# Performance work log

Measured on AMD Instinct MI355X. Metric: run time of the kernel, lower is better.

## Reference

```python
import jax, jax.numpy as jnp
import numpy as np

N, S, H, D = 2, 1024, 12, 64
HIDDEN = H * D
EPS = 1e-6


def setup_inputs() -> dict:
    key = jax.random.key(0)
    k1, k2, k3 = jax.random.split(key, 3)
    return {
        "q": jax.random.normal(k1, (N, S, H, D), dtype=jnp.float32),
        "v": jax.random.normal(k2, (N, S, H, D), dtype=jnp.float32),
        "attention_mask": jnp.ones((N, S), dtype=jnp.float32),
        "head_mask": jnp.ones((H,), dtype=jnp.float32),
        "pos_weight": jax.random.normal(k3, (S, HIDDEN), dtype=jnp.float32),
    }


def reference(q, v, attention_mask, head_mask, pos_weight):
    seq_len = q.shape[1]
    # transpose_for_scores: [S, hidden] -> [S, H, D]
    p = pos_weight[:seq_len].reshape(seq_len, H, D)
    # elu feature map: elu(x) + 1
    p = jax.nn.elu(p) + 1.0
    # broadcast to batch and apply padding mask: [N, S, H, D]
    p = p[None, :, :, :] * attention_mask[:, :, None, None]
    # pv: [N, H, M, D]
    pv = jnp.einsum('nshd,nshm->nhmd', p, v)
    pv = pv * head_mask[None, :, None, None]
    # ppv: [N, L, H, M, D]
    ppv = jnp.einsum('nlhd,nhmd->nlhmd', p, pv)
    # normalizer z_pp: [N, L, H]
    z_pp = jnp.einsum('nlhd,nhd->nlh', p, p.sum(axis=1)) + EPS
    return ppv, z_pp
```

## Files before the change

kernel.cpp:

```cpp
#include <hip/hip_runtime.h>
#include <math.h>

#define N_  2
#define S_  1024
#define H_  12
#define D_  64
#define HIDDEN_ 768
#define EPS_ 1e-6f

#define CHUNK 64
#define NS    (S_/CHUNK)

__device__ __forceinline__ float elup1(float x) {
    return x > 0.0f ? x + 1.0f : __expf(x);
}

__global__ __launch_bounds__(256) void pv_kernel(
        const float* __restrict__ v,
        const float* __restrict__ mask,
        const float* __restrict__ w,
        float* __restrict__ pv_part,
        float* __restrict__ psum_part) {
    __shared__ float p_lds[CHUNK * 64];
    __shared__ float v_lds[CHUNK * 64];

    const int b  = blockIdx.x;
    const int sc = b % NS;
    const int h  = (b / NS) % H_;
    const int n  = b / (NS * H_);
    const int s0 = sc * CHUNK;
    const int t  = threadIdx.x;

    for (int j = t; j < CHUNK * 16; j += 256) {
        const int row = j >> 4;
        const int c4  = (j & 15) * 4;
        const int s   = s0 + row;
        const float m = mask[n * S_ + s];
        const float4 wv = *(const float4*)(w + (size_t)s * HIDDEN_ + h * 64 + c4);
        float4 p;
        p.x = elup1(wv.x) * m;
        p.y = elup1(wv.y) * m;
        p.z = elup1(wv.z) * m;
        p.w = elup1(wv.w) * m;
        *(float4*)(p_lds + row * 64 + c4) = p;
        const float4 vv = *(const float4*)(v + (((size_t)n * S_ + s) * H_ + h) * 64 + c4);
        *(float4*)(v_lds + row * 64 + c4) = vv;
    }
    __syncthreads();

    const int d  = t & 63;
    const int mq = t >> 6;
    float acc[16];
    #pragma unroll
    for (int i = 0; i < 16; ++i) acc[i] = 0.0f;
    float ps = 0.0f;

    for (int s = 0; s < CHUNK; ++s) {
        const float pd = p_lds[s * 64 + d];
        ps += pd;
        const float* vr = v_lds + s * 64 + mq * 16;
        #pragma unroll
        for (int i = 0; i < 16; ++i)
            acc[i] = fmaf(pd, vr[i], acc[i]);
    }

    float* pvp = pv_part + (((size_t)(n * H_ + h)) * NS + sc) * (64 * 64);
    #pragma unroll
    for (int i = 0; i < 16; ++i)
        pvp[(mq * 16 + i) * 64 + d] = acc[i];
    if (mq == 0)
        psum_part[(((size_t)(n * H_ + h)) * NS + sc) * 64 + d] = ps;
}

__global__ __launch_bounds__(256) void reduce_kernel(
        const float* __restrict__ pv_part,
        const float* __restrict__ psum_part,
        float* __restrict__ pv_ws,
        float* __restrict__ psum_ws) {
    const int nh = blockIdx.x;
    const int t  = threadIdx.x;
    const float* src = pv_part + (size_t)nh * NS * 4096;
    float* dst = pv_ws + (size_t)nh * 4096;

    #pragma unroll
    for (int k = 0; k < 16; ++k) {
        const int e = t + k * 256;
        float s = 0.0f;
        #pragma unroll
        for (int sc = 0; sc < NS; ++sc)
            s += src[(size_t)sc * 4096 + e];
        dst[e] = s;
    }
    if (t < 64) {
        const float* ps = psum_part + (size_t)nh * NS * 64;
        float s = 0.0f;
        #pragma unroll
        for (int sc = 0; sc < NS; ++sc)
            s += ps[sc * 64 + t];
        psum_ws[nh * 64 + t] = s;
    }
}

__global__ __launch_bounds__(256) void ppv_kernel(
        const float* __restrict__ w,
        const float* __restrict__ mask,
        const float* __restrict__ head_mask,
        const float* __restrict__ pv_ws,
        const float* __restrict__ psum_ws,
        float* __restrict__ ppv_out,
        float* __restrict__ z_out) {
    __shared__ float p_l[64];

    const int b = blockIdx.x;
    const int h = b % H_;
    const int l = (b / H_) % S_;
    const int n = b / (H_ * S_);
    const int t = threadIdx.x;

    if (t < 64) {
        const float x = w[(size_t)l * HIDDEN_ + h * 64 + t];
        const float m = mask[n * S_ + l];
        const float p = elup1(x) * m;
        p_l[t] = p;
        float pz = p * psum_ws[(n * H_ + h) * 64 + t];
        #pragma unroll
        for (int off = 32; off > 0; off >>= 1)
            pz += __shfl_down(pz, off, 64);
        if (t == 0) z_out[b] = pz + EPS_;
    }
    __syncthreads();

    const float hm = head_mask[h];
    const float4* pv4 = (const float4*)(pv_ws + ((size_t)n * H_ + h) * (64 * 64));
    float4* out4 = (float4*)(ppv_out + (size_t)b * (64 * 64));

    #pragma unroll
    for (int jj = 0; jj < 4; ++jj) {
        const int j = t + jj * 256;
        const float4 vv = pv4[j];
        const float4 pw = *(const float4*)(p_l + ((j * 4) & 63));
        float4 r;
        r.x = pw.x * vv.x * hm;
        r.y = pw.y * vv.y * hm;
        r.z = pw.z * vv.z * hm;
        r.w = pw.w * vv.w * hm;
        out4[j] = r;
    }
}

extern "C" void kernel_launch(void* const* d_in, const int* in_sizes, int n_in,
                              void* d_out, int out_size, void* d_ws, size_t ws_size,
                              hipStream_t stream) {
    const float* v     = (const float*)d_in[1];
    const float* mask  = (const float*)d_in[2];
    const float* hmask = (const float*)d_in[3];
    const float* w     = (const float*)d_in[4];
    float* out = (float*)d_out;

    float* pv_part   = (float*)d_ws;
    float* psum_part = pv_part + (size_t)N_ * H_ * NS * 64 * 64;
    float* pv_ws     = psum_part + (size_t)N_ * H_ * NS * 64;
    float* psum_ws   = pv_ws + (size_t)N_ * H_ * 64 * 64;

    pv_kernel<<<dim3(N_ * H_ * NS), dim3(256), 0, stream>>>(
        v, mask, w, pv_part, psum_part);

    reduce_kernel<<<dim3(N_ * H_), dim3(256), 0, stream>>>(
        pv_part, psum_part, pv_ws, psum_ws);

    float* z_out = out + (size_t)N_ * S_ * H_ * 64 * 64;
    ppv_kernel<<<dim3(N_ * S_ * H_), dim3(256), 0, stream>>>(
        w, mask, hmask, pv_ws, psum_ws, out, z_out);
}
```

Baseline: 425.5 us.

## Tile ppv over 16 rows, reuse pv in registers, move z into reduce

```diff
diff --git a/kernel.cpp b/kernel.cpp
--- a/kernel.cpp
+++ b/kernel.cpp
@@ -10,6 +10,9 @@
 
 #define CHUNK 64
 #define NS    (S_/CHUNK)
+
+#define LT 16
+#define NL (S_/LT)
 
 __device__ __forceinline__ float elup1(float x) {
     return x > 0.0f ? x + 1.0f : __expf(x);
@@ -72,18 +75,35 @@
         psum_part[(((size_t)(n * H_ + h)) * NS + sc) * 64 + d] = ps;
 }
 
-__global__ __launch_bounds__(256) void reduce_kernel(
+__global__ __launch_bounds__(256) void reduce_z_kernel(
         const float* __restrict__ pv_part,
         const float* __restrict__ psum_part,
+        const float* __restrict__ w,
+        const float* __restrict__ mask,
         float* __restrict__ pv_ws,
-        float* __restrict__ psum_ws) {
-    const int nh = blockIdx.x;
+        float* __restrict__ z_out) {
+    __shared__ float psum_lds[64];
+
+    const int b  = blockIdx.x;
+    const int q  = b & 3;
+    const int h  = (b >> 2) % H_;
+    const int n  = b / (4 * H_);
+    const int nh = n * H_ + h;
     const int t  = threadIdx.x;
-    const float* src = pv_part + (size_t)nh * NS * 4096;
-    float* dst = pv_ws + (size_t)nh * 4096;
-
-    #pragma unroll
-    for (int k = 0; k < 16; ++k) {
+
+    if (t < 64) {
+        const float* ps = psum_part + (size_t)nh * NS * 64 + t;
+        float s = 0.0f;
+        #pragma unroll
+        for (int sc = 0; sc < NS; ++sc)
+            s += ps[sc * 64];
+        psum_lds[t] = s;
+    }
+
+    const float* src = pv_part + (size_t)nh * NS * 4096 + q * 1024;
+    float* dst = pv_ws + (size_t)nh * 4096 + q * 1024;
+    #pragma unroll
+    for (int k = 0; k < 4; ++k) {
         const int e = t + k * 256;
         float s = 0.0f;
         #pragma unroll
@@ -91,14 +111,21 @@
             s += src[(size_t)sc * 4096 + e];
         dst[e] = s;
     }
-    if (t < 64) {
-        const float* ps = psum_part + (size_t)nh * NS * 64;
-        float s = 0.0f;
-        #pragma unroll
-        for (int sc = 0; sc < NS; ++sc)
-            s += ps[sc * 64 + t];
-        psum_ws[nh * 64 + t] = s;
-    }
+    __syncthreads();
+
+    const int l = q * 256 + t;
+    const float m = mask[n * S_ + l];
+    const float4* wr = (const float4*)(w + (size_t)l * HIDDEN_ + h * 64);
+    float acc = 0.0f;
+    #pragma unroll
+    for (int i = 0; i < 16; ++i) {
+        const float4 wv = wr[i];
+        acc += elup1(wv.x) * psum_lds[i * 4 + 0];
+        acc += elup1(wv.y) * psum_lds[i * 4 + 1];
+        acc += elup1(wv.z) * psum_lds[i * 4 + 2];
+        acc += elup1(wv.w) * psum_lds[i * 4 + 3];
+    }
+    z_out[(n * S_ + l) * H_ + h] = acc * m + EPS_;
 }
 
 __global__ __launch_bounds__(256) void ppv_kernel(
@@ -106,45 +133,52 @@
         const float* __restrict__ mask,
         const float* __restrict__ head_mask,
         const float* __restrict__ pv_ws,
-        const float* __restrict__ psum_ws,
-        float* __restrict__ ppv_out,
-        float* __restrict__ z_out) {
-    __shared__ float p_l[64];
-
-    const int b = blockIdx.x;
-    const int h = b % H_;
-    const int l = (b / H_) % S_;
-    const int n = b / (H_ * S_);
-    const int t = threadIdx.x;
-
-    if (t < 64) {
-        const float x = w[(size_t)l * HIDDEN_ + h * 64 + t];
-        const float m = mask[n * S_ + l];
-        const float p = elup1(x) * m;
-        p_l[t] = p;
-        float pz = p * psum_ws[(n * H_ + h) * 64 + t];
-        #pragma unroll
-        for (int off = 32; off > 0; off >>= 1)
-            pz += __shfl_down(pz, off, 64);
-        if (t == 0) z_out[b] = pz + EPS_;
+        float* __restrict__ ppv_out) {
+    __shared__ float p_lds[LT * 64];
+
+    const int b  = blockIdx.x;
+    const int h  = b % H_;
+    const int lb = (b / H_) % NL;
+    const int n  = b / (H_ * NL);
+    const int l0 = lb * LT;
+    const int t  = threadIdx.x;
+
+    const float hm = head_mask[h];
+    const float4* pv4 = (const float4*)(pv_ws + ((size_t)(n * H_ + h)) * 4096);
+    float4 pr[4];
+    #pragma unroll
+    for (int jj = 0; jj < 4; ++jj) {
+        float4 vv = pv4[t + jj * 256];
+        vv.x *= hm; vv.y *= hm; vv.z *= hm; vv.w *= hm;
+        pr[jj] = vv;
+    }
+
+    const int d  = t & 63;
+    const int lw = t >> 6;
+    #pragma unroll
+    for (int lq = 0; lq < LT / 4; ++lq) {
+        const int l = lq * 4 + lw;
+        const float m = mask[n * S_ + l0 + l];
+        p_lds[l * 64 + d] =
+            elup1(w[(size_t)(l0 + l) * HIDDEN_ + h * 64 + d]) * m;
     }
     __syncthreads();
 
-    const float hm = head_mask[h];
-    const float4* pv4 = (const float4*)(pv_ws + ((size_t)n * H_ + h) * (64 * 64));
-    float4* out4 = (float4*)(ppv_out + (size_t)b * (64 * 64));
-
-    #pragma unroll
-    for (int jj = 0; jj < 4; ++jj) {
-        const int j = t + jj * 256;
-        const float4 vv = pv4[j];
-        const float4 pw = *(const float4*)(p_l + ((j * 4) & 63));
-        float4 r;
-        r.x = pw.x * vv.x * hm;
-        r.y = pw.y * vv.y * hm;
-        r.z = pw.z * vv.z * hm;
-        r.w = pw.w * vv.w * hm;
-        out4[j] = r;
+    const int d0 = (t * 4) & 63;
+    float4* outb = (float4*)ppv_out + ((size_t)(n * S_ + l0) * H_ + h) * 1024;
+    #pragma unroll 4
+    for (int l = 0; l < LT; ++l) {
+        const float4 pw = *(const float4*)(p_lds + l * 64 + d0);
+        float4* o = outb + (size_t)l * (H_ * 1024);
+        #pragma unroll
+        for (int jj = 0; jj < 4; ++jj) {
+            float4 r;
+            r.x = pw.x * pr[jj].x;
+            r.y = pw.y * pr[jj].y;
+            r.z = pw.z * pr[jj].z;
+            r.w = pw.w * pr[jj].w;
+            o[t + jj * 256] = r;
+        }
     }
 }
 
@@ -160,15 +194,15 @@
     float* pv_part   = (float*)d_ws;
     float* psum_part = pv_part + (size_t)N_ * H_ * NS * 64 * 64;
     float* pv_ws     = psum_part + (size_t)N_ * H_ * NS * 64;
-    float* psum_ws   = pv_ws + (size_t)N_ * H_ * 64 * 64;
+
+    float* z_out = out + (size_t)N_ * S_ * H_ * 64 * 64;
 
     pv_kernel<<<dim3(N_ * H_ * NS), dim3(256), 0, stream>>>(
         v, mask, w, pv_part, psum_part);
 
-    reduce_kernel<<<dim3(N_ * H_), dim3(256), 0, stream>>>(
-        pv_part, psum_part, pv_ws, psum_ws);
-
-    float* z_out = out + (size_t)N_ * S_ * H_ * 64 * 64;
-    ppv_kernel<<<dim3(N_ * S_ * H_), dim3(256), 0, stream>>>(
-        w, mask, hmask, pv_ws, psum_ws, out, z_out);
-}
+    reduce_z_kernel<<<dim3(N_ * H_ * 4), dim3(256), 0, stream>>>(
+        pv_part, psum_part, w, mask, pv_ws, z_out);
+
+    ppv_kernel<<<dim3(N_ * H_ * NL), dim3(256), 0, stream>>>(
+        w, mask, hmask, pv_ws, out);
+}
```

Result: no change. 432.2 us (+1.6%).
